# Kernel optimization log

Measured on AMD Instinct MI355X. Metric: run time of the kernel, lower is better.

Reference implementation:

```python
import jax, jax.numpy as jnp
import numpy as np

DIM = 256
HEADS = 4
HEAD_DIM = DIM // HEADS
SCALE = HEAD_DIM ** -0.5


def setup_inputs() -> dict:
    key = jax.random.key(0)
    ks = jax.random.split(key, 6)
    B, N, C = 4, 4096, DIM
    x = jax.random.normal(ks[0], (B, N, C), dtype=jnp.float32)
    # torch.nn.Linear weights are [out, in]; y = x @ W.T (+ b)
    s = 1.0 / np.sqrt(C)
    Wq = jax.random.uniform(ks[1], (C, C), jnp.float32, -s, s)
    Wk = jax.random.uniform(ks[2], (C, C), jnp.float32, -s, s)
    Wv = jax.random.uniform(ks[3], (C, C), jnp.float32, -s, s)
    Wp = jax.random.uniform(ks[4], (C, C), jnp.float32, -s, s)
    bp = jax.random.uniform(ks[5], (C,), jnp.float32, -s, s)
    return {"x": x, "Wq": Wq, "Wk": Wk, "Wv": Wv, "Wp": Wp, "bp": bp}


def reference(x, Wq, Wk, Wv, Wp, bp):
    B, N, C = x.shape
    H, D = HEADS, HEAD_DIM
    # project and split heads: [B, H, N, D]
    def heads(W):
        return (x @ W.T).reshape(B, N, H, D).transpose(0, 2, 1, 3)
    q = heads(Wq)
    k = heads(Wk)
    v = heads(Wv)
    attn = jnp.einsum('bhnd,bhmd->bhnm', q, k) * SCALE  # [B,H,N,N]
    attn = jax.nn.softmax(attn, axis=-1)
    out = jnp.einsum('bhnm,bhmd->bhnd', attn, v)  # [B,H,N,D]
    out = out.transpose(0, 2, 1, 3).reshape(B, N, C)
    return out @ Wp.T + bp
```

## Files before the change

kernel.cpp:

```cpp
#include <hip/hip_runtime.h>

typedef unsigned short u16t;
typedef unsigned int u32t;
typedef __bf16 bf16x8 __attribute__((ext_vector_type(8)));
typedef float f32x4 __attribute__((ext_vector_type(4)));
typedef float f32x16 __attribute__((ext_vector_type(16)));
typedef unsigned int u32x4 __attribute__((ext_vector_type(4)));
typedef unsigned int u32x2 __attribute__((ext_vector_type(2)));

#define DEV static __device__ __forceinline__

DEV u16t f2bf(float f){
  u32t u = __builtin_bit_cast(u32t, f);
  u += 0x7fffu + ((u >> 16) & 1u);
  return (u16t)(u >> 16);
}

DEV u32t cvtpk(float lo, float hi){
  u32t r;
  asm("v_cvt_pk_bf16_f32 %0, %1, %2" : "=v"(r) : "v"(lo), "v"(hi));
  return r;
}

DEV void plswap(u32t &a, u32t &b){
  asm("v_permlane32_swap_b32 %0, %1" : "+v"(a), "+v"(b));
}

DEV float fexp2(float x){
#if __has_builtin(__builtin_amdgcn_exp2f)
  return __builtin_amdgcn_exp2f(x);
#else
  return exp2f(x);
#endif
}

DEV void gll16(const void* g, void* l){
  __builtin_amdgcn_global_load_lds((const __attribute__((address_space(1))) void*)g,
                                   (__attribute__((address_space(3))) void*)l, 16, 0, 0);
}

DEV f32x4 mfma16(bf16x8 a, bf16x8 b, f32x4 c){
  return __builtin_amdgcn_mfma_f32_16x16x32_bf16(a, b, c, 0, 0, 0);
}

DEV f32x16 mfma32(bf16x8 a, bf16x8 b, f32x16 c){
  return __builtin_amdgcn_mfma_f32_32x32x16_bf16(a, b, c, 0, 0, 0);
}

__global__ __launch_bounds__(256) void k_cast_x(const float4* __restrict__ x, u16t* __restrict__ xb){
  int idx = blockIdx.x * 256 + threadIdx.x;
  float4 v = x[idx];
  ushort4 o = make_ushort4(f2bf(v.x), f2bf(v.y), f2bf(v.z), f2bf(v.w));
  *(ushort4*)&xb[idx * 4] = o;
}

__global__ __launch_bounds__(256) void k_cast_w(const float* __restrict__ Wq, const float* __restrict__ Wk,
                         const float* __restrict__ Wv, const float* __restrict__ Wp,
                         u16t* __restrict__ wqkv, u16t* __restrict__ wp){
  int idx = blockIdx.x * 256 + threadIdx.x;
  if (idx < 196608){
    float v;
    if (idx < 65536)        v = Wq[idx] * 0.1803368801f;
    else if (idx < 131072)  v = Wk[idx - 65536];
    else                    v = Wv[idx - 131072];
    wqkv[idx] = f2bf(v);
  } else {
    int j = idx - 196608;
    wp[j] = f2bf(Wp[j]);
  }
}

template<bool IS_QKV>
__global__ __launch_bounds__(256) void k_gemm(const u16t* __restrict__ A, const u16t* __restrict__ W,
    const float* __restrict__ bias, u16t* __restrict__ oq, u16t* __restrict__ okk, u16t* __restrict__ vtg,
    float* __restrict__ op, int Ntot){
  __shared__ u32x4 sm[1536];
  const int tid = threadIdx.x, lane = tid & 63, w = tid >> 6, g = lane >> 4, li = lane & 15;
  const int m0 = blockIdx.x * 128, n0 = blockIdx.y * 64;
  const int wm = w >> 1, wn = w & 1;
  f32x4 acc[4][2] = {};
  for (int kk = 0; kk < 4; ++kk){
    #pragma unroll
    for (int rnd = 0; rnd < 4; ++rnd){
      int cid = rnd * 256 + tid;
      int row = cid >> 3, ch = cid & 7;
      const u16t* src = A + (m0 + row) * 256 + kk * 64 + ((ch ^ (row & 7)) << 3);
      gll16(src, (char*)sm + (rnd * 256 + w * 64) * 16);
    }
    #pragma unroll
    for (int rnd = 0; rnd < 2; ++rnd){
      int cid = rnd * 256 + tid;
      int row = cid >> 3, ch = cid & 7;
      const u16t* src = W + (n0 + row) * 256 + kk * 64 + ((ch ^ (row & 7)) << 3);
      gll16(src, (char*)sm + 16384 + (rnd * 256 + w * 64) * 16);
    }
    __syncthreads();
    #pragma unroll
    for (int ks = 0; ks < 2; ++ks){
      bf16x8 bfr[2];
      #pragma unroll
      for (int nj = 0; nj < 2; ++nj){
        int row = wn * 32 + nj * 16 + li;
        bfr[nj] = __builtin_bit_cast(bf16x8, sm[1024 + row * 8 + ((ks * 4 + g) ^ (row & 7))]);
      }
      #pragma unroll
      for (int mi = 0; mi < 4; ++mi){
        int row = wm * 64 + mi * 16 + li;
        bf16x8 af = __builtin_bit_cast(bf16x8, sm[row * 8 + ((ks * 4 + g) ^ (row & 7))]);
        #pragma unroll
        for (int nj = 0; nj < 2; ++nj)
          acc[mi][nj] = mfma16(af, bfr[nj], acc[mi][nj]);
      }
    }
    __syncthreads();
  }
  if (IS_QKV){
    const int which = n0 >> 8, h = (n0 >> 6) & 3;
    if (which == 2){
      u16t* smv = (u16t*)sm;
      #pragma unroll
      for (int mi = 0; mi < 4; ++mi){
        #pragma unroll
        for (int nj = 0; nj < 2; ++nj){
          int d = wn * 32 + nj * 16 + li;
          int mloc = wm * 64 + mi * 16 + g * 4;
          u32x2 pk2;
          pk2.x = cvtpk(acc[mi][nj][0], acc[mi][nj][1]);
          pk2.y = cvtpk(acc[mi][nj][2], acc[mi][nj][3]);
          int chk = mloc >> 3, inner = (mloc & 7) * 2;
          *(u32x2*)((char*)smv + d * 256 + (((chk ^ (d & 7))) << 4) + inner) = pk2;
        }
      }
      __syncthreads();
      const int b = m0 >> 12, bh2 = b * 4 + h, mbase = m0 & 4095;
      #pragma unroll
      for (int rnd = 0; rnd < 4; ++rnd){
        int qq = rnd * 256 + tid;
        int d = qq >> 4, ch = qq & 15;
        *(u32x4*)&vtg[((size_t)bh2 * 64 + d) * 4096 + mbase + ch * 8] =
            *(const u32x4*)((char*)smv + d * 256 + ((ch ^ (d & 7)) << 4));
      }
    } else {
      u16t* outp = which == 0 ? oq : okk;
      #pragma unroll
      for (int mi = 0; mi < 4; ++mi){
        int m = m0 + wm * 64 + mi * 16 + g * 4;
        int b = m >> 12, nn = m & 4095;
        #pragma unroll
        for (int nj = 0; nj < 2; ++nj){
          int d = wn * 32 + nj * 16 + li;
          #pragma unroll
          for (int r = 0; r < 4; ++r)
            outp[((b * 4 + h) * 4096 + nn + r) * 64 + d] = f2bf(acc[mi][nj][r]);
        }
      }
    }
  } else {
    #pragma unroll
    for (int mi = 0; mi < 4; ++mi){
      int m = m0 + wm * 64 + mi * 16 + g * 4;
      #pragma unroll
      for (int nj = 0; nj < 2; ++nj){
        int n = n0 + wn * 32 + nj * 16 + li;
        float bv = bias[n];
        #pragma unroll
        for (int r = 0; r < 4; ++r)
          op[(m + r) * Ntot + n] = acc[mi][nj][r] + bv;
      }
    }
  }
}

__global__ __launch_bounds__(128, 2) void k_flash(const u16t* __restrict__ q,
    const u16t* __restrict__ kg, const u16t* __restrict__ vtg, u16t* __restrict__ ao){
  __shared__ u32x4 sm4[2080];
  char* sm = (char*)sm4;
  const int tid = threadIdx.x, lane = tid & 63, w = tid >> 6;
  const int hi = lane >> 5, p = lane & 31;
  const int bid = blockIdx.x;
  const int swz = (bid & 7) * 128 + (bid >> 3);
  const int bh = swz >> 6, qt = swz & 63;
  const int rowbase = qt * 64;
  const u16t* kb = kg + (size_t)bh * 262144 + (size_t)w * 2048 * 64;
  const u16t* vb = vtg + (size_t)bh * 262144 + w * 2048;
  char* Kb = sm + w * 16384;
  char* Vb = Kb + 8192;

  u32x4 qf[2][4];
  #pragma unroll
  for (int it = 0; it < 2; ++it)
    #pragma unroll
    for (int kk = 0; kk < 4; ++kk)
      qf[it][kk] = *(const u32x4*)&q[((size_t)bh * 4096 + rowbase + it * 32 + p) * 64 + kk * 16 + hi * 8];

  f32x16 ot[2][2] = {};
  float lsp[2][4] = {};

  auto stageK = [&](int t){
    #pragma unroll
    for (int i = 0; i < 8; ++i){
      int cid = i * 64 + lane;
      int row = cid >> 3, ch = cid & 7;
      gll16(kb + (t * 64 + row) * 64 + ((ch ^ (row & 7)) << 3), Kb + cid * 16);
    }
  };
  auto stageV = [&](int t){
    #pragma unroll
    for (int i = 0; i < 8; ++i){
      int cid = i * 64 + lane;
      int row = cid >> 3, ch = cid & 7;
      gll16(vb + row * 4096 + t * 64 + ((ch ^ (row & 7)) << 3), Vb + cid * 16);
    }
  };

  stageK(0);
  stageV(0);
  #pragma unroll 1
  for (int t = 0; t < 32; ++t){
    asm volatile("s_waitcnt vmcnt(8)" ::: "memory");
    f32x16 st[2][2] = {};
    #pragma unroll
    for (int kk = 0; kk < 4; ++kk)
      #pragma unroll
      for (int jt = 0; jt < 2; ++jt){
        int row = jt * 32 + p;
        bf16x8 kf = __builtin_bit_cast(bf16x8,
            *(const u32x4*)(Kb + row * 128 + (((kk * 2 + hi) ^ (row & 7)) << 4)));
        st[0][jt] = mfma32(kf, __builtin_bit_cast(bf16x8, qf[0][kk]), st[0][jt]);
        st[1][jt] = mfma32(kf, __builtin_bit_cast(bf16x8, qf[1][kk]), st[1][jt]);
      }
    asm volatile("s_waitcnt lgkmcnt(0)" ::: "memory");
    stageK((t + 1) & 31);
    u32x4 pf[2][2][2];
    #pragma unroll
    for (int it = 0; it < 2; ++it)
      #pragma unroll
      for (int jt = 0; jt < 2; ++jt){
        float e[16];
        #pragma unroll
        for (int r = 0; r < 16; ++r)
          e[r] = fexp2(st[it][jt][r]);
        #pragma unroll
        for (int r = 0; r < 16; ++r)
          lsp[it][r & 3] += e[r];
        #pragma unroll
        for (int s = 0; s < 2; ++s){
          u32t a0 = cvtpk(e[s*8+0], e[s*8+1]);
          u32t a1 = cvtpk(e[s*8+2], e[s*8+3]);
          u32t b0 = cvtpk(e[s*8+4], e[s*8+5]);
          u32t b1 = cvtpk(e[s*8+6], e[s*8+7]);
          plswap(a0, b0);
          plswap(a1, b1);
          pf[it][jt][s] = (u32x4){a0, a1, b0, b1};
        }
      }
    asm volatile("s_waitcnt vmcnt(8)" ::: "memory");
    #pragma unroll
    for (int jt = 0; jt < 2; ++jt)
      #pragma unroll
      for (int s = 0; s < 2; ++s)
        #pragma unroll
        for (int dt = 0; dt < 2; ++dt){
          int row = dt * 32 + p;
          bf16x8 vf = __builtin_bit_cast(bf16x8,
              *(const u32x4*)(Vb + row * 128 + ((((jt * 2 + s) * 2 + hi) ^ (row & 7)) << 4)));
          ot[0][dt] = mfma32(vf, __builtin_bit_cast(bf16x8, pf[0][jt][s]), ot[0][dt]);
          ot[1][dt] = mfma32(vf, __builtin_bit_cast(bf16x8, pf[1][jt][s]), ot[1][dt]);
        }
    asm volatile("s_waitcnt lgkmcnt(0)" ::: "memory");
    stageV((t + 1) & 31);
  }
  asm volatile("s_waitcnt vmcnt(0) lgkmcnt(0)" ::: "memory");

  float l4[2];
  #pragma unroll
  for (int it = 0; it < 2; ++it){
    float v = (lsp[it][0] + lsp[it][1]) + (lsp[it][2] + lsp[it][3]);
    v += __shfl_xor(v, 32);
    l4[it] = v;
  }
  __syncthreads();

  char* reg = sm + w * 16384;
  #pragma unroll
  for (int it = 0; it < 2; ++it)
    #pragma unroll
    for (int dt = 0; dt < 2; ++dt)
      #pragma unroll
      for (int s = 0; s < 4; ++s){
        f32x4 v4 = {ot[it][dt][4*s+0], ot[it][dt][4*s+1], ot[it][dt][4*s+2], ot[it][dt][4*s+3]};
        int quad = 2 * s + hi + 8 * dt;
        *(f32x4*)(reg + it * 8192 + p * 256 + ((quad ^ (p & 15)) << 4)) = v4;
      }
  float* lsums = (float*)(sm + 32768);
  if (lane < 32){
    lsums[(w * 2 + 0) * 32 + lane] = l4[0];
    lsums[(w * 2 + 1) * 32 + lane] = l4[1];
  }
  __syncthreads();

  {
    const int qloc = lane >> 1, dh = lane & 1;
    float ltot = lsums[(0 * 2 + w) * 32 + qloc] + lsums[(1 * 2 + w) * 32 + qloc];
    float inv = __builtin_amdgcn_rcpf(ltot);
    const int b = bh >> 2, h = bh & 3;
    u16t* dst = ao + ((size_t)b * 4096 + rowbase + w * 32 + qloc) * 256 + h * 64 + dh * 32;
    u32t pk[16];
    #pragma unroll
    for (int k = 0; k < 8; ++k){
      int quad = dh * 8 + k;
      f32x4 a = *(const f32x4*)(sm + 0 * 16384 + w * 8192 + qloc * 256 + ((quad ^ (qloc & 15)) << 4));
      f32x4 c = *(const f32x4*)(sm + 1 * 16384 + w * 8192 + qloc * 256 + ((quad ^ (qloc & 15)) << 4));
      f32x4 o = (a + c) * inv;
      pk[2*k]   = cvtpk(o[0], o[1]);
      pk[2*k+1] = cvtpk(o[2], o[3]);
    }
    #pragma unroll
    for (int k = 0; k < 4; ++k)
      *(u32x4*)(dst + k * 8) = (u32x4){pk[4*k], pk[4*k+1], pk[4*k+2], pk[4*k+3]};
  }
}

extern "C" void kernel_launch(void* const* d_in, const int* in_sizes, int n_in,
                              void* d_out, int out_size, void* d_ws, size_t ws_size,
                              hipStream_t stream){
  (void)in_sizes; (void)n_in; (void)out_size; (void)ws_size;
  const float* x  = (const float*)d_in[0];
  const float* Wq = (const float*)d_in[1];
  const float* Wk = (const float*)d_in[2];
  const float* Wv = (const float*)d_in[3];
  const float* Wp = (const float*)d_in[4];
  const float* bp = (const float*)d_in[5];
  float* out = (float*)d_out;

  u16t* ws   = (u16t*)d_ws;
  u16t* xb   = ws;
  u16t* qg   = ws + 4194304;
  u16t* kg   = ws + 8388608;
  u16t* vtg  = ws + 12582912;
  u16t* ao   = ws + 16777216;
  u16t* wqkv = ws + 20971520;
  u16t* wpb  = ws + 21168128;

  k_cast_x<<<4096, 256, 0, stream>>>((const float4*)x, xb);
  k_cast_w<<<1024, 256, 0, stream>>>(Wq, Wk, Wv, Wp, wqkv, wpb);
  k_gemm<true><<<dim3(128, 12), 256, 0, stream>>>(xb, wqkv, nullptr, qg, kg, vtg, nullptr, 768);
  k_flash<<<1024, 128, 0, stream>>>(qg, kg, vtg, ao);
  k_gemm<false><<<dim3(128, 4), 256, 0, stream>>>(ao, wpb, bp, nullptr, nullptr, nullptr, out, 256);
}
```

Before: 111.5 us.

## Load K directly into registers and double-buffer pre-tiled V in LDS

The projection kernel now writes V-transpose in a tiled, pre-swizzled layout so each 64x64 tile is contiguous. The flash kernel reads K fragments straight from global memory into registers one tile ahead, and double-buffers V tiles in LDS. QK^T for the next tile is issued right after PV under raised wave priority, to overlap the loads with compute. This removes K's LDS staging and the per-tile LDS waits, at the cost of more registers. The final iteration prefetches past the end of the K/V buffers.

```diff
diff --git a/kernel.cpp b/kernel.cpp
--- a/kernel.cpp
+++ b/kernel.cpp
@@ -137,8 +137,10 @@
       for (int rnd = 0; rnd < 4; ++rnd){
         int qq = rnd * 256 + tid;
         int d = qq >> 4, ch = qq & 15;
-        *(u32x4*)&vtg[((size_t)bh2 * 64 + d) * 4096 + mbase + ch * 8] =
-            *(const u32x4*)((char*)smv + d * 256 + ((ch ^ (d & 7)) << 4));
+        u32x4 val = *(const u32x4*)((char*)smv + d * 256 + ((ch ^ (d & 7)) << 4));
+        int nt = (mbase >> 6) + (ch >> 3);
+        int cs = (ch & 7) ^ (d & 7);
+        *(u32x4*)&vtg[((size_t)(bh2 * 64 + nt) * 64 + d) * 64 + cs * 8] = val;
       }
     } else {
       u16t* outp = which == 0 ? oq : okk;
@@ -172,19 +174,21 @@
 }
 
 __global__ __launch_bounds__(128, 2) void k_flash(const u16t* __restrict__ q,
-    const u16t* __restrict__ kg, const u16t* __restrict__ vtg, u16t* __restrict__ ao){
-  __shared__ u32x4 sm4[2080];
-  char* sm = (char*)sm4;
+    const u16t* __restrict__ kg, const u16t* __restrict__ vt, u16t* __restrict__ ao){
+  __shared__ char sm[33280];
   const int tid = threadIdx.x, lane = tid & 63, w = tid >> 6;
   const int hi = lane >> 5, p = lane & 31;
   const int bid = blockIdx.x;
   const int swz = (bid & 7) * 128 + (bid >> 3);
   const int bh = swz >> 6, qt = swz & 63;
   const int rowbase = qt * 64;
-  const u16t* kb = kg + (size_t)bh * 262144 + (size_t)w * 2048 * 64;
-  const u16t* vb = vtg + (size_t)bh * 262144 + w * 2048;
-  char* Kb = sm + w * 16384;
-  char* Vb = Kb + 8192;
+
+  const char* kp0 = (const char*)(kg + (size_t)bh * 262144 + (size_t)w * 131072) + p * 128 + hi * 16;
+  const char* kp1 = kp0 + 4096;
+  const char* vp0 = (const char*)vt + (size_t)bh * 524288 + (size_t)w * 262144 + (size_t)lane * 16;
+  const char* vp1 = vp0 + 4096;
+  char* Vb0 = sm + w * 16384;
+  char* Vb1 = Vb0 + 8192;
 
   u32x4 qf[2][4];
   #pragma unroll
@@ -195,42 +199,39 @@
 
   f32x16 ot[2][2] = {};
   float lsp[2][4] = {};
-
-  auto stageK = [&](int t){
-    #pragma unroll
-    for (int i = 0; i < 8; ++i){
-      int cid = i * 64 + lane;
-      int row = cid >> 3, ch = cid & 7;
-      gll16(kb + (t * 64 + row) * 64 + ((ch ^ (row & 7)) << 3), Kb + cid * 16);
-    }
-  };
-  auto stageV = [&](int t){
-    #pragma unroll
-    for (int i = 0; i < 8; ++i){
-      int cid = i * 64 + lane;
-      int row = cid >> 3, ch = cid & 7;
-      gll16(vb + row * 4096 + t * 64 + ((ch ^ (row & 7)) << 3), Vb + cid * 16);
-    }
-  };
-
-  stageK(0);
-  stageV(0);
+  u32x4 kreg[2][4];
+  f32x16 st[2][2];
+  const f32x16 fz = {};
+
+  #pragma unroll
+  for (int jt = 0; jt < 2; ++jt)
+    #pragma unroll
+    for (int kk = 0; kk < 4; ++kk)
+      kreg[jt][kk] = *(const u32x4*)((jt ? kp1 : kp0) + kk * 32);
+  kp0 += 8192; kp1 += 8192;
+  #pragma unroll
+  for (int i = 0; i < 8; ++i)
+    gll16((i < 4 ? vp0 : vp1) + (i & 3) * 1024, Vb0 + i * 1024 + lane * 16);
+  vp0 += 8192; vp1 += 8192;
+  #pragma unroll
+  for (int jt = 0; jt < 2; ++jt)
+    #pragma unroll
+    for (int it = 0; it < 2; ++it){
+      f32x16 a = mfma32(__builtin_bit_cast(bf16x8, kreg[jt][0]), __builtin_bit_cast(bf16x8, qf[it][0]), fz);
+      a = mfma32(__builtin_bit_cast(bf16x8, kreg[jt][1]), __builtin_bit_cast(bf16x8, qf[it][1]), a);
+      a = mfma32(__builtin_bit_cast(bf16x8, kreg[jt][2]), __builtin_bit_cast(bf16x8, qf[it][2]), a);
+      a = mfma32(__builtin_bit_cast(bf16x8, kreg[jt][3]), __builtin_bit_cast(bf16x8, qf[it][3]), a);
+      st[it][jt] = a;
+    }
+  #pragma unroll
+  for (int jt = 0; jt < 2; ++jt)
+    #pragma unroll
+    for (int kk = 0; kk < 4; ++kk)
+      kreg[jt][kk] = *(const u32x4*)((jt ? kp1 : kp0) + kk * 32);
+  kp0 += 8192; kp1 += 8192;
+
   #pragma unroll 1
   for (int t = 0; t < 32; ++t){
-    asm volatile("s_waitcnt vmcnt(8)" ::: "memory");
-    f32x16 st[2][2] = {};
-    #pragma unroll
-    for (int kk = 0; kk < 4; ++kk)
-      #pragma unroll
-      for (int jt = 0; jt < 2; ++jt){
-        int row = jt * 32 + p;
-        bf16x8 kf = __builtin_bit_cast(bf16x8,
-            *(const u32x4*)(Kb + row * 128 + (((kk * 2 + hi) ^ (row & 7)) << 4)));
-        st[0][jt] = mfma32(kf, __builtin_bit_cast(bf16x8, qf[0][kk]), st[0][jt]);
-        st[1][jt] = mfma32(kf, __builtin_bit_cast(bf16x8, qf[1][kk]), st[1][jt]);
-      }
-    asm volatile("s_waitcnt lgkmcnt(0)" ::: "memory");
-    stageK((t + 1) & 31);
     u32x4 pf[2][2][2];
     #pragma unroll
     for (int it = 0; it < 2; ++it)
@@ -255,6 +256,8 @@
         }
       }
     asm volatile("s_waitcnt vmcnt(8)" ::: "memory");
+    const char* vbcur = (t & 1) ? Vb1 : Vb0;
+    __builtin_amdgcn_s_setprio(1);
     #pragma unroll
     for (int jt = 0; jt < 2; ++jt)
       #pragma unroll
@@ -263,14 +266,34 @@
         for (int dt = 0; dt < 2; ++dt){
           int row = dt * 32 + p;
           bf16x8 vf = __builtin_bit_cast(bf16x8,
-              *(const u32x4*)(Vb + row * 128 + ((((jt * 2 + s) * 2 + hi) ^ (row & 7)) << 4)));
+              *(const u32x4*)(vbcur + row * 128 + ((((jt * 2 + s) * 2 + hi) ^ (row & 7)) << 4)));
           ot[0][dt] = mfma32(vf, __builtin_bit_cast(bf16x8, pf[0][jt][s]), ot[0][dt]);
           ot[1][dt] = mfma32(vf, __builtin_bit_cast(bf16x8, pf[1][jt][s]), ot[1][dt]);
         }
-    asm volatile("s_waitcnt lgkmcnt(0)" ::: "memory");
-    stageV((t + 1) & 31);
-  }
-  asm volatile("s_waitcnt vmcnt(0) lgkmcnt(0)" ::: "memory");
+    #pragma unroll
+    for (int jt = 0; jt < 2; ++jt)
+      #pragma unroll
+      for (int it = 0; it < 2; ++it){
+        f32x16 a = mfma32(__builtin_bit_cast(bf16x8, kreg[jt][0]), __builtin_bit_cast(bf16x8, qf[it][0]), fz);
+        a = mfma32(__builtin_bit_cast(bf16x8, kreg[jt][1]), __builtin_bit_cast(bf16x8, qf[it][1]), a);
+        a = mfma32(__builtin_bit_cast(bf16x8, kreg[jt][2]), __builtin_bit_cast(bf16x8, qf[it][2]), a);
+        a = mfma32(__builtin_bit_cast(bf16x8, kreg[jt][3]), __builtin_bit_cast(bf16x8, qf[it][3]), a);
+        st[it][jt] = a;
+      }
+    __builtin_amdgcn_s_setprio(0);
+    char* vbn = (t & 1) ? Vb0 : Vb1;
+    #pragma unroll
+    for (int i = 0; i < 8; ++i)
+      gll16((i < 4 ? vp0 : vp1) + (i & 3) * 1024, vbn + i * 1024 + lane * 16);
+    vp0 += 8192; vp1 += 8192;
+    #pragma unroll
+    for (int jt = 0; jt < 2; ++jt)
+      #pragma unroll
+      for (int kk = 0; kk < 4; ++kk)
+        kreg[jt][kk] = *(const u32x4*)((jt ? kp1 : kp0) + kk * 32);
+    kp0 += 8192; kp1 += 8192;
+  }
+  asm volatile("s_waitcnt vmcnt(0)" ::: "memory");
 
   float l4[2];
   #pragma unroll
```

Measured after the change: 118.1 us. 5.9% more time.

## Split flash attention key range across four waves instead of two

Applied to the files above, without the earlier changes.

The flash kernel now runs 256 threads (4 waves) per block. Each wave handles a quarter of the keys using 32-key tiles, with a reworked V-tile layout and swizzle, instead of two waves each taking half the keys in 64-key tiles. The four partial outputs and row sums are reduced through shared memory in two passes over the query sub-tiles. This is meant to raise occupancy and latency hiding and to lower per-wave register pressure, at the cost of more barriers, a larger cross-wave reduction, and smaller MFMA batches per iteration.

```diff
diff --git a/kernel.cpp b/kernel.cpp
--- a/kernel.cpp
+++ b/kernel.cpp
@@ -171,20 +171,19 @@
   }
 }
 
-__global__ __launch_bounds__(128, 2) void k_flash(const u16t* __restrict__ q,
+__global__ __launch_bounds__(256, 4) void k_flash(const u16t* __restrict__ q,
     const u16t* __restrict__ kg, const u16t* __restrict__ vtg, u16t* __restrict__ ao){
-  __shared__ u32x4 sm4[2080];
-  char* sm = (char*)sm4;
+  __shared__ char sm[33792];
   const int tid = threadIdx.x, lane = tid & 63, w = tid >> 6;
   const int hi = lane >> 5, p = lane & 31;
   const int bid = blockIdx.x;
   const int swz = (bid & 7) * 128 + (bid >> 3);
   const int bh = swz >> 6, qt = swz & 63;
   const int rowbase = qt * 64;
-  const u16t* kb = kg + (size_t)bh * 262144 + (size_t)w * 2048 * 64;
-  const u16t* vb = vtg + (size_t)bh * 262144 + w * 2048;
-  char* Kb = sm + w * 16384;
-  char* Vb = Kb + 8192;
+  const u16t* kb = kg + (size_t)bh * 262144 + (size_t)w * 65536;
+  const u16t* vb = vtg + (size_t)bh * 262144 + w * 1024;
+  char* Kb = sm + w * 8192;
+  char* Vb = Kb + 4096;
 
   u32x4 qf[2][4];
   #pragma unroll
@@ -195,21 +194,22 @@
 
   f32x16 ot[2][2] = {};
   float lsp[2][4] = {};
+  const f32x16 fz = {};
 
   auto stageK = [&](int t){
     #pragma unroll
-    for (int i = 0; i < 8; ++i){
+    for (int i = 0; i < 4; ++i){
       int cid = i * 64 + lane;
       int row = cid >> 3, ch = cid & 7;
-      gll16(kb + (t * 64 + row) * 64 + ((ch ^ (row & 7)) << 3), Kb + cid * 16);
+      gll16(kb + (t * 32 + row) * 64 + ((ch ^ (row & 7)) << 3), Kb + cid * 16);
     }
   };
   auto stageV = [&](int t){
     #pragma unroll
-    for (int i = 0; i < 8; ++i){
+    for (int i = 0; i < 4; ++i){
       int cid = i * 64 + lane;
-      int row = cid >> 3, ch = cid & 7;
-      gll16(vb + row * 4096 + t * 64 + ((ch ^ (row & 7)) << 3), Vb + cid * 16);
+      int d = cid >> 2, c = cid & 3;
+      gll16(vb + d * 4096 + t * 32 + ((c ^ ((d >> 1) & 3)) << 3), Vb + cid * 16);
     }
   };
 
@@ -217,107 +217,108 @@
   stageV(0);
   #pragma unroll 1
   for (int t = 0; t < 32; ++t){
-    asm volatile("s_waitcnt vmcnt(8)" ::: "memory");
-    f32x16 st[2][2] = {};
-    #pragma unroll
-    for (int kk = 0; kk < 4; ++kk)
-      #pragma unroll
-      for (int jt = 0; jt < 2; ++jt){
-        int row = jt * 32 + p;
-        bf16x8 kf = __builtin_bit_cast(bf16x8,
-            *(const u32x4*)(Kb + row * 128 + (((kk * 2 + hi) ^ (row & 7)) << 4)));
-        st[0][jt] = mfma32(kf, __builtin_bit_cast(bf16x8, qf[0][kk]), st[0][jt]);
-        st[1][jt] = mfma32(kf, __builtin_bit_cast(bf16x8, qf[1][kk]), st[1][jt]);
-      }
+    asm volatile("s_waitcnt vmcnt(4)" ::: "memory");
+    f32x16 st0, st1;
+    #pragma unroll
+    for (int kk = 0; kk < 4; ++kk){
+      bf16x8 kf = __builtin_bit_cast(bf16x8,
+          *(const u32x4*)(Kb + p * 128 + (((kk * 2 + hi) ^ (p & 7)) << 4)));
+      if (kk == 0){
+        st0 = mfma32(kf, __builtin_bit_cast(bf16x8, qf[0][0]), fz);
+        st1 = mfma32(kf, __builtin_bit_cast(bf16x8, qf[1][0]), fz);
+      } else {
+        st0 = mfma32(kf, __builtin_bit_cast(bf16x8, qf[0][kk]), st0);
+        st1 = mfma32(kf, __builtin_bit_cast(bf16x8, qf[1][kk]), st1);
+      }
+    }
     asm volatile("s_waitcnt lgkmcnt(0)" ::: "memory");
     stageK((t + 1) & 31);
-    u32x4 pf[2][2][2];
-    #pragma unroll
-    for (int it = 0; it < 2; ++it)
-      #pragma unroll
-      for (int jt = 0; jt < 2; ++jt){
-        float e[16];
-        #pragma unroll
-        for (int r = 0; r < 16; ++r)
-          e[r] = fexp2(st[it][jt][r]);
-        #pragma unroll
-        for (int r = 0; r < 16; ++r)
-          lsp[it][r & 3] += e[r];
-        #pragma unroll
-        for (int s = 0; s < 2; ++s){
-          u32t a0 = cvtpk(e[s*8+0], e[s*8+1]);
-          u32t a1 = cvtpk(e[s*8+2], e[s*8+3]);
-          u32t b0 = cvtpk(e[s*8+4], e[s*8+5]);
-          u32t b1 = cvtpk(e[s*8+6], e[s*8+7]);
-          plswap(a0, b0);
-          plswap(a1, b1);
-          pf[it][jt][s] = (u32x4){a0, a1, b0, b1};
-        }
-      }
-    asm volatile("s_waitcnt vmcnt(8)" ::: "memory");
-    #pragma unroll
-    for (int jt = 0; jt < 2; ++jt)
-      #pragma unroll
-      for (int s = 0; s < 2; ++s)
-        #pragma unroll
-        for (int dt = 0; dt < 2; ++dt){
-          int row = dt * 32 + p;
-          bf16x8 vf = __builtin_bit_cast(bf16x8,
-              *(const u32x4*)(Vb + row * 128 + ((((jt * 2 + s) * 2 + hi) ^ (row & 7)) << 4)));
-          ot[0][dt] = mfma32(vf, __builtin_bit_cast(bf16x8, pf[0][jt][s]), ot[0][dt]);
-          ot[1][dt] = mfma32(vf, __builtin_bit_cast(bf16x8, pf[1][jt][s]), ot[1][dt]);
-        }
+    u32x4 pf[2][2];
+    #pragma unroll
+    for (int it = 0; it < 2; ++it){
+      const f32x16& s = it ? st1 : st0;
+      float e[16];
+      #pragma unroll
+      for (int r = 0; r < 16; ++r)
+        e[r] = fexp2(s[r]);
+      #pragma unroll
+      for (int r = 0; r < 16; ++r)
+        lsp[it][r & 3] += e[r];
+      #pragma unroll
+      for (int sx = 0; sx < 2; ++sx){
+        u32t a0 = cvtpk(e[sx*8+0], e[sx*8+1]);
+        u32t a1 = cvtpk(e[sx*8+2], e[sx*8+3]);
+        u32t b0 = cvtpk(e[sx*8+4], e[sx*8+5]);
+        u32t b1 = cvtpk(e[sx*8+6], e[sx*8+7]);
+        plswap(a0, b0);
+        plswap(a1, b1);
+        pf[it][sx] = (u32x4){a0, a1, b0, b1};
+      }
+    }
+    asm volatile("s_waitcnt vmcnt(4)" ::: "memory");
+    #pragma unroll
+    for (int sx = 0; sx < 2; ++sx)
+      #pragma unroll
+      for (int dt = 0; dt < 2; ++dt){
+        int d = dt * 32 + p;
+        bf16x8 vf = __builtin_bit_cast(bf16x8,
+            *(const u32x4*)(Vb + d * 64 + (((sx * 2 + hi) ^ ((d >> 1) & 3)) << 4)));
+        ot[0][dt] = mfma32(vf, __builtin_bit_cast(bf16x8, pf[0][sx]), ot[0][dt]);
+        ot[1][dt] = mfma32(vf, __builtin_bit_cast(bf16x8, pf[1][sx]), ot[1][dt]);
+      }
     asm volatile("s_waitcnt lgkmcnt(0)" ::: "memory");
     stageV((t + 1) & 31);
   }
-  asm volatile("s_waitcnt vmcnt(0) lgkmcnt(0)" ::: "memory");
-
-  float l4[2];
-  #pragma unroll
+  asm volatile("s_waitcnt vmcnt(0)" ::: "memory");
+
+  float* lsums = (float*)(sm + 32768);
+  {
+    float l0 = (lsp[0][0] + lsp[0][1]) + (lsp[0][2] + lsp[0][3]);
+    float l1 = (lsp[1][0] + lsp[1][1]) + (lsp[1][2] + lsp[1][3]);
+    l0 += __shfl_xor(l0, 32);
+    l1 += __shfl_xor(l1, 32);
+    if (lane < 32){
+      lsums[(w * 2 + 0) * 32 + lane] = l0;
+      lsums[(w * 2 + 1) * 32 + lane] = l1;
+    }
+  }
+  __syncthreads();
+
+  const int b = bh >> 2, h = bh & 3;
+  #pragma unroll 1
   for (int it = 0; it < 2; ++it){
-    float v = (lsp[it][0] + lsp[it][1]) + (lsp[it][2] + lsp[it][3]);
-    v += __shfl_xor(v, 32);
-    l4[it] = v;
-  }
-  __syncthreads();
-
-  char* reg = sm + w * 16384;
-  #pragma unroll
-  for (int it = 0; it < 2; ++it)
+    char* reg = sm + w * 8192;
     #pragma unroll
     for (int dt = 0; dt < 2; ++dt)
       #pragma unroll
-      for (int s = 0; s < 4; ++s){
-        f32x4 v4 = {ot[it][dt][4*s+0], ot[it][dt][4*s+1], ot[it][dt][4*s+2], ot[it][dt][4*s+3]};
-        int quad = 2 * s + hi + 8 * dt;
-        *(f32x4*)(reg + it * 8192 + p * 256 + ((quad ^ (p & 15)) << 4)) = v4;
-      }
-  float* lsums = (float*)(sm + 32768);
-  if (lane < 32){
-    lsums[(w * 2 + 0) * 32 + lane] = l4[0];
-    lsums[(w * 2 + 1) * 32 + lane] = l4[1];
-  }
-  __syncthreads();
-
-  {
-    const int qloc = lane >> 1, dh = lane & 1;
-    float ltot = lsums[(0 * 2 + w) * 32 + qloc] + lsums[(1 * 2 + w) * 32 + qloc];
-    float inv = __builtin_amdgcn_rcpf(ltot);
-    const int b = bh >> 2, h = bh & 3;
-    u16t* dst = ao + ((size_t)b * 4096 + rowbase + w * 32 + qloc) * 256 + h * 64 + dh * 32;
-    u32t pk[16];
-    #pragma unroll
-    for (int k = 0; k < 8; ++k){
-      int quad = dh * 8 + k;
-      f32x4 a = *(const f32x4*)(sm + 0 * 16384 + w * 8192 + qloc * 256 + ((quad ^ (qloc & 15)) << 4));
-      f32x4 c = *(const f32x4*)(sm + 1 * 16384 + w * 8192 + qloc * 256 + ((quad ^ (qloc & 15)) << 4));
-      f32x4 o = (a + c) * inv;
-      pk[2*k]   = cvtpk(o[0], o[1]);
-      pk[2*k+1] = cvtpk(o[2], o[3]);
-    }
-    #pragma unroll
-    for (int k = 0; k < 4; ++k)
-      *(u32x4*)(dst + k * 8) = (u32x4){pk[4*k], pk[4*k+1], pk[4*k+2], pk[4*k+3]};
+      for (int s4 = 0; s4 < 4; ++s4){
+        f32x4 v4 = {ot[it][dt][4*s4+0], ot[it][dt][4*s4+1], ot[it][dt][4*s4+2], ot[it][dt][4*s4+3]};
+        int quad = 2 * s4 + hi + 8 * dt;
+        *(f32x4*)(reg + p * 256 + ((quad ^ (p & 15)) << 4)) = v4;
+      }
+    __syncthreads();
+    {
+      const int qloc = tid >> 3, ck = tid & 7;
+      float ltot = lsums[(0 * 2 + it) * 32 + qloc] + lsums[(1 * 2 + it) * 32 + qloc]
+                 + lsums[(2 * 2 + it) * 32 + qloc] + lsums[(3 * 2 + it) * 32 + qloc];
+      float inv = __builtin_amdgcn_rcpf(ltot);
+      u32t pk[4];
+      #pragma unroll
+      for (int k2 = 0; k2 < 2; ++k2){
+        int quad = ck * 2 + k2;
+        int off = qloc * 256 + ((quad ^ (qloc & 15)) << 4);
+        f32x4 s = *(const f32x4*)(sm + 0 * 8192 + off);
+        s = s + *(const f32x4*)(sm + 1 * 8192 + off);
+        s = s + *(const f32x4*)(sm + 2 * 8192 + off);
+        s = s + *(const f32x4*)(sm + 3 * 8192 + off);
+        s = s * inv;
+        pk[2*k2]   = cvtpk(s[0], s[1]);
+        pk[2*k2+1] = cvtpk(s[2], s[3]);
+      }
+      *(u32x4*)&ao[((size_t)b * 4096 + rowbase + it * 32 + qloc) * 256 + h * 64 + ck * 8] =
+          (u32x4){pk[0], pk[1], pk[2], pk[3]};
+    }
+    __syncthreads();
   }
 }
 
@@ -345,6 +346,6 @@
   k_cast_x<<<4096, 256, 0, stream>>>((const float4*)x, xb);
   k_cast_w<<<1024, 256, 0, stream>>>(Wq, Wk, Wv, Wp, wqkv, wpb);
   k_gemm<true><<<dim3(128, 12), 256, 0, stream>>>(xb, wqkv, nullptr, qg, kg, vtg, nullptr, 768);
-  k_flash<<<1024, 128, 0, stream>>>(qg, kg, vtg, ao);
+  k_flash<<<1024, 256, 0, stream>>>(qg, kg, vtg, ao);
   k_gemm<false><<<dim3(128, 4), 256, 0, stream>>>(ao, wpb, bp, nullptr, nullptr, nullptr, out, 256);
 }
```

Result: slower. 334.1 us (+199.6%).

## Pre-tile V^T in MFMA fragment order and add setprio around MFMA blocks

Applied to the files above, without the earlier changes.

The projection kernel now writes V^T in a tiled layout: 64-key tiles, 16-byte chunks ordered by chunk index then head-dim row. The flash kernel can therefore stage each V tile with fully contiguous 1KB loads and read fragments without XOR swizzle arithmetic. This is meant to cut strided global gathers and address math in the inner loop. It also raises wave priority during the MFMA sections so they interleave better with the other wave, which has to be tuned carefully.

```diff
diff --git a/kernel.cpp b/kernel.cpp
--- a/kernel.cpp
+++ b/kernel.cpp
@@ -136,9 +136,10 @@
       #pragma unroll
       for (int rnd = 0; rnd < 4; ++rnd){
         int qq = rnd * 256 + tid;
-        int d = qq >> 4, ch = qq & 15;
-        *(u32x4*)&vtg[((size_t)bh2 * 64 + d) * 4096 + mbase + ch * 8] =
-            *(const u32x4*)((char*)smv + d * 256 + ((ch ^ (d & 7)) << 4));
+        int d = qq & 63, cidx = qq >> 6;
+        u32x4 val = *(const u32x4*)((char*)smv + d * 256 + ((cidx ^ (d & 7)) << 4));
+        int nt = (mbase >> 6) + (cidx >> 3), i = cidx & 7;
+        *(u32x4*)((char*)vtg + ((((size_t)bh2 * 64 + nt) * 8 + i) * 64 + d) * 16) = val;
       }
     } else {
       u16t* outp = which == 0 ? oq : okk;
@@ -172,7 +173,7 @@
 }
 
 __global__ __launch_bounds__(128, 2) void k_flash(const u16t* __restrict__ q,
-    const u16t* __restrict__ kg, const u16t* __restrict__ vtg, u16t* __restrict__ ao){
+    const u16t* __restrict__ kg, const u16t* __restrict__ vt, u16t* __restrict__ ao){
   __shared__ u32x4 sm4[2080];
   char* sm = (char*)sm4;
   const int tid = threadIdx.x, lane = tid & 63, w = tid >> 6;
@@ -181,8 +182,9 @@
   const int swz = (bid & 7) * 128 + (bid >> 3);
   const int bh = swz >> 6, qt = swz & 63;
   const int rowbase = qt * 64;
-  const u16t* kb = kg + (size_t)bh * 262144 + (size_t)w * 2048 * 64;
-  const u16t* vb = vtg + (size_t)bh * 262144 + w * 2048;
+  const u16t* kb = kg + (size_t)bh * 262144 + (size_t)w * 131072;
+  const char* vbB = (const char*)vt + (size_t)bh * 524288 + (size_t)w * 262144
+                    + (size_t)lane * 16;
   char* Kb = sm + w * 16384;
   char* Vb = Kb + 8192;
 
@@ -206,11 +208,8 @@
   };
   auto stageV = [&](int t){
     #pragma unroll
-    for (int i = 0; i < 8; ++i){
-      int cid = i * 64 + lane;
-      int row = cid >> 3, ch = cid & 7;
-      gll16(vb + row * 4096 + t * 64 + ((ch ^ (row & 7)) << 3), Vb + cid * 16);
-    }
+    for (int i = 0; i < 8; ++i)
+      gll16(vbB + (size_t)t * 8192 + i * 1024, Vb + i * 1024 + lane * 16);
   };
 
   stageK(0);
@@ -218,6 +217,7 @@
   #pragma unroll 1
   for (int t = 0; t < 32; ++t){
     asm volatile("s_waitcnt vmcnt(8)" ::: "memory");
+    __builtin_amdgcn_s_setprio(1);
     f32x16 st[2][2] = {};
     #pragma unroll
     for (int kk = 0; kk < 4; ++kk)
@@ -229,6 +229,7 @@
         st[0][jt] = mfma32(kf, __builtin_bit_cast(bf16x8, qf[0][kk]), st[0][jt]);
         st[1][jt] = mfma32(kf, __builtin_bit_cast(bf16x8, qf[1][kk]), st[1][jt]);
       }
+    __builtin_amdgcn_s_setprio(0);
     asm volatile("s_waitcnt lgkmcnt(0)" ::: "memory");
     stageK((t + 1) & 31);
     u32x4 pf[2][2][2];
@@ -255,22 +256,23 @@
         }
       }
     asm volatile("s_waitcnt vmcnt(8)" ::: "memory");
+    __builtin_amdgcn_s_setprio(1);
     #pragma unroll
     for (int jt = 0; jt < 2; ++jt)
       #pragma unroll
       for (int s = 0; s < 2; ++s)
         #pragma unroll
         for (int dt = 0; dt < 2; ++dt){
-          int row = dt * 32 + p;
           bf16x8 vf = __builtin_bit_cast(bf16x8,
-              *(const u32x4*)(Vb + row * 128 + ((((jt * 2 + s) * 2 + hi) ^ (row & 7)) << 4)));
+              *(const u32x4*)(Vb + (jt * 2 + s) * 2048 + hi * 1024 + dt * 512 + p * 16));
           ot[0][dt] = mfma32(vf, __builtin_bit_cast(bf16x8, pf[0][jt][s]), ot[0][dt]);
           ot[1][dt] = mfma32(vf, __builtin_bit_cast(bf16x8, pf[1][jt][s]), ot[1][dt]);
         }
+    __builtin_amdgcn_s_setprio(0);
     asm volatile("s_waitcnt lgkmcnt(0)" ::: "memory");
     stageV((t + 1) & 31);
   }
-  asm volatile("s_waitcnt vmcnt(0) lgkmcnt(0)" ::: "memory");
+  asm volatile("s_waitcnt vmcnt(0)" ::: "memory");
 
   float l4[2];
   #pragma unroll
```

Measured after the change: 112.7 us. Within noise of the previous version (+1.1%).
